# Kernel optimization log

Hardware: AMD Instinct MI355X
Metric: run time of the kernel (lower is better)

Reference implementation:

```python
import jax, jax.numpy as jnp
import numpy as np

B, LQ, LK = 8, 1024, 1024
H, HD = 8, 128            # n_head, hidden_dim (per-head)
HEAD_DIM, CHILD_DIM = 512, 512
D_MODEL = HEAD_DIM + CHILD_DIM
TEMP = float(np.sqrt(HD))
NEG = 100000000.0
EPS = 1e-5


def setup_inputs() -> dict:
    key = jax.random.key(0)
    ks = jax.random.split(key, 12)
    q = jax.random.normal(ks[0], (B, LQ, HEAD_DIM), jnp.float32)
    k = jax.random.normal(ks[1], (B, LK, CHILD_DIM), jnp.float32)
    v = jax.random.normal(ks[2], (B, LK, D_MODEL), jnp.float32)
    old_score = 0.1 * jax.random.normal(ks[3], (H * B, LQ, LK), jnp.float32)
    float_mask = (jax.random.uniform(ks[4], (B, LQ, LK)) > 0.2).astype(jnp.float32)
    # torch nn.Linear weights are [out_features, in_features]
    wq = jax.random.normal(ks[5], (H * HD, HEAD_DIM), jnp.float32) * np.sqrt(2.0 / (HEAD_DIM + HD))
    wk = jax.random.normal(ks[6], (H * HD, CHILD_DIM), jnp.float32) * np.sqrt(2.0 / (CHILD_DIM + HD))
    wv = jax.random.normal(ks[7], (H * HD, D_MODEL), jnp.float32) * np.sqrt(2.0 / (D_MODEL + HD))
    wfc = jax.random.normal(ks[8], (D_MODEL, H * HD), jnp.float32) * np.sqrt(2.0 / (D_MODEL + H * HD))
    bq = jnp.zeros((H * HD,), jnp.float32)
    bk = jnp.zeros((H * HD,), jnp.float32)
    bv = jnp.zeros((H * HD,), jnp.float32)
    bfc = jnp.zeros((D_MODEL,), jnp.float32)
    ln_g = jnp.ones((D_MODEL,), jnp.float32)
    ln_b = jnp.zeros((D_MODEL,), jnp.float32)
    return dict(q=q, k=k, v=v, old_score=old_score, float_mask=float_mask,
                wq=wq, bq=bq, wk=wk, bk=bk, wv=wv, bv=bv,
                wfc=wfc, bfc=bfc, ln_g=ln_g, ln_b=ln_b)


def reference(q, k, v, old_score, float_mask, wq, bq, wk, bk, wv, bv, wfc, bfc, ln_g, ln_b):
    b, lq, _ = q.shape
    lk = k.shape[1]
    residual = v
    qh = (q @ wq.T + bq).reshape(b, lq, H, HD)   # [b,lq,h,d]
    kh = (k @ wk.T + bk).reshape(b, lk, H, HD)
    vh = (v @ wv.T + bv).reshape(b, lk, H, HD)
    # raw_score laid out head-major to match torch's (n_head*B, Lq, Lk)
    raw = jnp.einsum('bqhd,bkhd->hbqk', qh, kh) + old_score.reshape(H, b, lq, lk)
    score = raw - NEG * (1.0 - float_mask)[None]          # broadcast over heads
    attn = jax.nn.softmax(score / TEMP, axis=-1)          # eval path
    out = jnp.einsum('hbqk,bkhd->bqhd', attn, vh).reshape(b, lq, H * HD)
    out = out @ wfc.T + bfc + residual                    # dropout=identity (eval)
    mean = jnp.mean(out, axis=-1, keepdims=True)
    var = jnp.mean(jnp.square(out - mean), axis=-1, keepdims=True)
    out = (out - mean) / jnp.sqrt(var + EPS) * ln_g + ln_b
    return out, raw.reshape(H * b, lq, lk)
```

## Files before the change

kernel.cpp:

```cpp
#include <hip/hip_runtime.h>

typedef unsigned short u16;
typedef __bf16 bf16x8 __attribute__((ext_vector_type(8)));
typedef float f32x4 __attribute__((ext_vector_type(4)));

#define MFMA16(a,b,c) __builtin_amdgcn_mfma_f32_16x16x32_bf16(a,b,c,0,0,0)

static __device__ __forceinline__ u16 f2bf(float f){
  unsigned u = __builtin_bit_cast(unsigned, f);
  u += 0x7fffu + ((u>>16)&1u);
  return (u16)(u>>16);
}
static __device__ __forceinline__ int swz256(int r,int c){ return r*256 + (c ^ ((r&7)<<4)); }
static __device__ __forceinline__ int swz128(int r,int c){ return r*128 + (c ^ ((r&7)<<4)); }

static __device__ __forceinline__ void gload16(const void* g, void* l){
  __builtin_amdgcn_global_load_lds(
      (const __attribute__((address_space(1))) unsigned int*)g,
      (__attribute__((address_space(3))) unsigned int*)l, 16, 0, 0);
}

__global__ void conv_f2b(const float* __restrict__ in, u16* __restrict__ out, int n4){
  int i = blockIdx.x*256 + threadIdx.x;
  if (i >= n4) return;
  float4 f = reinterpret_cast<const float4*>(in)[i];
  ushort4 o; o.x=f2bf(f.x); o.y=f2bf(f.y); o.z=f2bf(f.z); o.w=f2bf(f.w);
  reinterpret_cast<ushort4*>(out)[i] = o;
}

template<int MODE>
__global__ __launch_bounds__(256) void gemm_nt(const u16* __restrict__ A, const u16* __restrict__ Bw,
    const float* __restrict__ bias, const float* __restrict__ resid,
    u16* __restrict__ Cb, float* __restrict__ Cf, int M, int N, int K)
{
  __shared__ uint4 ldsv[2048];
  char* la = (char*)ldsv;
  char* lb = la + 16384;
  const int tid = threadIdx.x, lane = tid&63, w = tid>>6;
  const int l15 = lane&15, l4 = lane>>4;
  const int wm = w&1, wn = w>>1;
  const int mb = blockIdx.x, nb = blockIdx.y;
  const f32x4 zero4 = {0.f,0.f,0.f,0.f};
  f32x4 acc[4][4];
  #pragma unroll
  for (int i=0;i<4;++i)
    #pragma unroll
    for (int j=0;j<4;++j) acc[i][j] = zero4;

  for (int k0=0;k0<K;k0+=64){
    __syncthreads();
    #pragma unroll
    for (int it=0; it<4; ++it){
      int slot = it*256 + tid;
      int r = slot>>3, cg = (slot&7) ^ (r&7);
      gload16(A + (size_t)(mb*128+r)*K + k0 + cg*8, la + (it*256 + w*64)*16);
      gload16(Bw + (size_t)(nb*128+r)*K + k0 + cg*8, lb + (it*256 + w*64)*16);
    }
    __syncthreads();
    #pragma unroll
    for (int kk=0;kk<2;++kk){
      bf16x8 af[4], bfr[4];
      #pragma unroll
      for (int i=0;i<4;++i){
        af[i]  = *reinterpret_cast<const bf16x8*>(la + swz128(wm*64+i*16+l15, (kk*32+l4*8)*2));
        bfr[i] = *reinterpret_cast<const bf16x8*>(lb + swz128(wn*64+i*16+l15, (kk*32+l4*8)*2));
      }
      #pragma unroll
      for (int i=0;i<4;++i)
        #pragma unroll
        for (int j=0;j<4;++j)
          acc[i][j] = MFMA16(af[i], bfr[j], acc[i][j]);
    }
  }
  #pragma unroll
  for (int j=0;j<4;++j){
    int col = nb*128 + wn*64 + j*16 + l15;
    float bv = bias[col];
    #pragma unroll
    for (int i=0;i<4;++i){
      int row0 = mb*128 + wm*64 + i*16 + l4*4;
      if (MODE == 0){
        #pragma unroll
        for (int r=0;r<4;++r)
          Cb[(size_t)(row0+r)*N + col] = f2bf(acc[i][j][r] + bv);
      } else if (MODE == 1){
        int bb = row0 >> 10, kp = row0 & 1023;
        ushort4 o;
        o.x = f2bf(acc[i][j][0]+bv); o.y = f2bf(acc[i][j][1]+bv);
        o.z = f2bf(acc[i][j][2]+bv); o.w = f2bf(acc[i][j][3]+bv);
        *reinterpret_cast<ushort4*>(Cb + (size_t)(bb*1024+col)*1024 + kp) = o;
      } else {
        #pragma unroll
        for (int r=0;r<4;++r){
          size_t off = (size_t)(row0+r)*N + col;
          Cf[off] = acc[i][j][r] + bv + resid[off];
        }
      }
    }
  }
}

__global__ __launch_bounds__(256) void attn_fused(const u16* __restrict__ qh,
    const u16* __restrict__ kh, const u16* __restrict__ vt,
    const float* __restrict__ oldsc, const float* __restrict__ fmask,
    float* __restrict__ raw, u16* __restrict__ ao)
{
  __shared__ uint4 ldsv[4608];
  char* lk0 = (char*)ldsv;
  char* lv0 = lk0 + 16384;
  char* lk1 = lk0 + 32768;
  char* lv1 = lk0 + 49152;
  char* lp_ = lk0 + 65536;
  const int tid = threadIdx.x, lane = tid&63, w = tid>>6;
  const int l15 = lane&15, l4 = lane>>4;
  const int qb = blockIdx.x, b = blockIdx.y, h = blockIdx.z;
  const float invT = 0.088388347648318447f;
  const f32x4 zero4 = {0.f,0.f,0.f,0.f};

  const int qglob = qb*64 + w*16 + l4*4;
  const float* oldp = oldsc + ((size_t)(h*8+b)*1024 + qglob)*1024 + l15*4;
  const float* fmp  = fmask + ((size_t)b*1024 + qglob)*1024 + l15*4;
  float*       rawp = raw   + ((size_t)(h*8+b)*1024 + qglob)*1024 + l15*4;
  const u16* khB = kh + (size_t)b*1024*1024 + h*128;
  const u16* vtB = vt + ((size_t)b*1024 + h*128)*1024;

  bf16x8 qf[4];
  {
    const u16* qp = qh + (size_t)(b*1024 + qb*64 + w*16 + l15)*1024 + h*128 + l4*8;
    #pragma unroll
    for (int kk=0;kk<4;++kk)
      qf[kk] = __builtin_bit_cast(bf16x8, *reinterpret_cast<const uint4*>(qp + kk*32));
  }
  f32x4 oacc[8];
  #pragma unroll
  for (int i=0;i<8;++i) oacc[i] = zero4;
  float mr[4], lr[4];
  #pragma unroll
  for (int r=0;r<4;++r){ mr[r] = -3.0e38f; lr[r] = 0.f; }

  auto stage = [&](int kt, char* lkD, char* lvD){
    #pragma unroll
    for (int it=0; it<4; ++it){
      int slot = it*256 + tid;
      int rs = slot>>4, cs = slot&15;
      int cgk = cs ^ (rs&7);
      int kv = (rs&15)*4 + (rs>>4);
      gload16(khB + (size_t)(kt*64 + kv)*1024 + cgk*8, lkD + (it*256 + w*64)*16);
      int r8 = slot>>3, cgv = (slot&7) ^ (r8&7);
      gload16(vtB + (size_t)r8*1024 + kt*64 + cgv*8, lvD + (it*256 + w*64)*16);
    }
  };
  auto pref = [&](int kt, float4 (&o4)[4], float4 (&m4)[4]){
    #pragma unroll
    for (int r=0;r<4;++r){
      o4[r] = *reinterpret_cast<const float4*>(oldp + (size_t)r*1024 + kt*64);
      m4[r] = *reinterpret_cast<const float4*>(fmp  + (size_t)r*1024 + kt*64);
    }
  };
  auto body = [&](int kt, char* lkR, char* lvR, float4 (&o4)[4], float4 (&m4)[4]){
    f32x4 fs[4];
    #pragma unroll
    for (int fj=0;fj<4;++fj){
      f32x4 s = zero4;
      #pragma unroll
      for (int kk=0;kk<4;++kk){
        bf16x8 kf = *reinterpret_cast<const bf16x8*>(lkR + swz256(fj*16+l15, (kk*32+l4*8)*2));
        s = MFMA16(qf[kk], kf, s);
      }
      fs[fj] = s;
    }
    float tm[4];
    #pragma unroll
    for (int r=0;r<4;++r){
      float4 rv;
      rv.x = fs[0][r] + o4[r].x; rv.y = fs[1][r] + o4[r].y;
      rv.z = fs[2][r] + o4[r].z; rv.w = fs[3][r] + o4[r].w;
      *reinterpret_cast<float4*>(rawp + (size_t)r*1024 + kt*64) = rv;
      fs[0][r] = (rv.x - 1.0e8f*(1.0f - m4[r].x)) * invT;
      fs[1][r] = (rv.y - 1.0e8f*(1.0f - m4[r].y)) * invT;
      fs[2][r] = (rv.z - 1.0e8f*(1.0f - m4[r].z)) * invT;
      fs[3][r] = (rv.w - 1.0e8f*(1.0f - m4[r].w)) * invT;
      tm[r] = fmaxf(fmaxf(fs[0][r], fs[1][r]), fmaxf(fs[2][r], fs[3][r]));
    }
    #pragma unroll
    for (int o=1;o<16;o<<=1){
      #pragma unroll
      for (int r=0;r<4;++r) tm[r] = fmaxf(tm[r], __shfl_xor(tm[r], o));
    }
    #pragma unroll
    for (int r=0;r<4;++r){
      float mn  = fmaxf(mr[r], tm[r]);
      float esc = __expf(mr[r] - mn);
      mr[r] = mn;
      lr[r] *= esc;
      #pragma unroll
      for (int nf=0;nf<8;++nf) oacc[nf][r] *= esc;
      float px = __expf(fs[0][r] - mn), py = __expf(fs[1][r] - mn);
      float pz = __expf(fs[2][r] - mn), pw = __expf(fs[3][r] - mn);
      lr[r] += px + py + pz + pw;
      ushort4 o;
      o.x = f2bf(px); o.y = f2bf(py); o.z = f2bf(pz); o.w = f2bf(pw);
      int prow = w*16 + l4*4 + r;
      *reinterpret_cast<ushort4*>(lp_ + swz128(prow, l15*8)) = o;
    }
    #pragma unroll
    for (int kkv=0;kkv<2;++kkv){
      bf16x8 pf = *reinterpret_cast<const bf16x8*>(lp_ + swz128(w*16+l15, (kkv*32+l4*8)*2));
      #pragma unroll
      for (int nf=0;nf<8;++nf){
        bf16x8 vf = *reinterpret_cast<const bf16x8*>(lvR + swz128(nf*16+l15, (kkv*32+l4*8)*2));
        oacc[nf] = MFMA16(pf, vf, oacc[nf]);
      }
    }
    __syncthreads();
  };

  float4 oA[4], mA[4], oB[4], mB[4];
  stage(0, lk0, lv0);
  pref(0, oA, mA);
  __syncthreads();
  for (int kt=0; kt<16; kt+=2){
    stage(kt+1, lk1, lv1);
    pref(kt+1, oB, mB);
    body(kt, lk0, lv0, oA, mA);
    if (kt+2 < 16){ stage(kt+2, lk0, lv0); pref(kt+2, oA, mA); }
    body(kt+1, lk1, lv1, oB, mB);
  }

  #pragma unroll
  for (int o=1;o<16;o<<=1){
    #pragma unroll
    for (int r=0;r<4;++r) lr[r] += __shfl_xor(lr[r], o);
  }
  #pragma unroll
  for (int nf=0;nf<8;++nf){
    int col = h*128 + nf*16 + l15;
    #pragma unroll
    for (int r=0;r<4;++r){
      size_t orow = (size_t)(b*1024 + qb*64 + w*16 + l4*4 + r);
      ao[orow*1024 + col] = f2bf(oacc[nf][r] * (1.0f/lr[r]));
    }
  }
}

__global__ __launch_bounds__(256) void ln_k(float* __restrict__ io,
    const float* __restrict__ g, const float* __restrict__ bb)
{
  const int lane = threadIdx.x & 63, w = threadIdx.x >> 6;
  size_t row = (size_t)blockIdx.x*4 + w;
  float4* p = reinterpret_cast<float4*>(io + row*1024);
  float4 x[4];
  float s = 0.f, s2 = 0.f;
  #pragma unroll
  for (int i=0;i<4;++i){
    x[i] = p[lane + i*64];
    s  += x[i].x + x[i].y + x[i].z + x[i].w;
    s2 += x[i].x*x[i].x + x[i].y*x[i].y + x[i].z*x[i].z + x[i].w*x[i].w;
  }
  #pragma unroll
  for (int o=1;o<64;o<<=1){ s += __shfl_xor(s,o); s2 += __shfl_xor(s2,o); }
  float mean = s * 0.0009765625f;
  float var  = s2 * 0.0009765625f - mean*mean;
  float rstd = rsqrtf(var + 1e-5f);
  const float4* gp = reinterpret_cast<const float4*>(g);
  const float4* bp = reinterpret_cast<const float4*>(bb);
  #pragma unroll
  for (int i=0;i<4;++i){
    float4 gg = gp[lane+i*64], bv = bp[lane+i*64], y;
    y.x = (x[i].x-mean)*rstd*gg.x + bv.x;
    y.y = (x[i].y-mean)*rstd*gg.y + bv.y;
    y.z = (x[i].z-mean)*rstd*gg.z + bv.z;
    y.w = (x[i].w-mean)*rstd*gg.w + bv.w;
    p[lane+i*64] = y;
  }
}

extern "C" void kernel_launch(void* const* d_in, const int* in_sizes, int n_in,
                              void* d_out, int out_size, void* d_ws, size_t ws_size,
                              hipStream_t stream)
{
  const float* q    = (const float*)d_in[0];
  const float* k    = (const float*)d_in[1];
  const float* v    = (const float*)d_in[2];
  const float* olds = (const float*)d_in[3];
  const float* fm   = (const float*)d_in[4];
  const float* wq   = (const float*)d_in[5];
  const float* bq   = (const float*)d_in[6];
  const float* wk   = (const float*)d_in[7];
  const float* bk   = (const float*)d_in[8];
  const float* wv   = (const float*)d_in[9];
  const float* bv   = (const float*)d_in[10];
  const float* wfc  = (const float*)d_in[11];
  const float* bfc  = (const float*)d_in[12];
  const float* lng  = (const float*)d_in[13];
  const float* lnb  = (const float*)d_in[14];
  float* out = (float*)d_out;
  float* raw = out + 8388608;

  u16* ws  = (u16*)d_ws;
  u16* qbf = ws;
  u16* kbf = qbf + 4194304;
  u16* vbf = kbf + 4194304;
  u16* wqb = vbf + 8388608;
  u16* wkb = wqb + 524288;
  u16* wvb = wkb + 524288;
  u16* wfb = wvb + 1048576;
  u16* qhb = wfb + 1048576;
  u16* khb = qhb + 8388608;
  u16* vtb = khb + 8388608;
  u16* aob = vtb + 8388608;

  conv_f2b<<<4096,256,0,stream>>>(q,   qbf, 1048576);
  conv_f2b<<<4096,256,0,stream>>>(k,   kbf, 1048576);
  conv_f2b<<<8192,256,0,stream>>>(v,   vbf, 2097152);
  conv_f2b<<<512, 256,0,stream>>>(wq,  wqb, 131072);
  conv_f2b<<<512, 256,0,stream>>>(wk,  wkb, 131072);
  conv_f2b<<<1024,256,0,stream>>>(wv,  wvb, 262144);
  conv_f2b<<<1024,256,0,stream>>>(wfc, wfb, 262144);

  gemm_nt<0><<<dim3(64,8),256,0,stream>>>(qbf, wqb, bq, nullptr, qhb, nullptr, 8192,1024,512);
  gemm_nt<0><<<dim3(64,8),256,0,stream>>>(kbf, wkb, bk, nullptr, khb, nullptr, 8192,1024,512);
  gemm_nt<1><<<dim3(64,8),256,0,stream>>>(vbf, wvb, bv, nullptr, vtb, nullptr, 8192,1024,1024);

  attn_fused<<<dim3(16,8,8),256,0,stream>>>(qhb, khb, vtb, olds, fm, raw, aob);

  gemm_nt<2><<<dim3(64,8),256,0,stream>>>(aob, wfb, bfc, v, nullptr, out, 8192,1024,1024);
  ln_k<<<2048,256,0,stream>>>(out, lng, lnb);
}
```

Baseline: 313.2 us.

## Pack attention mask to bits, remap blocks, and pipeline attention with explicit waits

A new kernel packs the float mask into one bit per element, so the attention kernel reads one byte per 8 mask values instead of float4 loads, which cuts mask traffic inside attention. The attention grid becomes 1D, with a block-index remap so blocks sharing the same (b,h) are grouped across XCDs for K/V cache reuse. The main loop is rewritten with explicit vmcnt waits, raw barriers and sched_barriers so the next tile's loads stay in flight while the current tile computes, replacing full __syncthreads. The cost is an extra pass over the mask plus more fragile manual synchronisation.

```diff
diff --git a/kernel.cpp b/kernel.cpp
--- a/kernel.cpp
+++ b/kernel.cpp
@@ -5,6 +5,9 @@
 typedef float f32x4 __attribute__((ext_vector_type(4)));
 
 #define MFMA16(a,b,c) __builtin_amdgcn_mfma_f32_16x16x32_bf16(a,b,c,0,0,0)
+#define WAITV(n) asm volatile("s_waitcnt vmcnt(" #n ")" ::: "memory")
+#define SBAR()   __builtin_amdgcn_s_barrier()
+#define SCHED0() __builtin_amdgcn_sched_barrier(0)
 
 static __device__ __forceinline__ u16 f2bf(float f){
   unsigned u = __builtin_bit_cast(unsigned, f);
@@ -26,6 +29,22 @@
   float4 f = reinterpret_cast<const float4*>(in)[i];
   ushort4 o; o.x=f2bf(f.x); o.y=f2bf(f.y); o.z=f2bf(f.z); o.w=f2bf(f.w);
   reinterpret_cast<ushort4*>(out)[i] = o;
+}
+
+__global__ void mask2bits(const float* __restrict__ fm, unsigned char* __restrict__ bits){
+  int i = blockIdx.x*256 + threadIdx.x;
+  const float4* p = reinterpret_cast<const float4*>(fm + (size_t)i*8);
+  float4 a = p[0], bq = p[1];
+  unsigned v = 0;
+  v |= (a.x  > 0.5f) ? 1u   : 0u;
+  v |= (a.y  > 0.5f) ? 2u   : 0u;
+  v |= (a.z  > 0.5f) ? 4u   : 0u;
+  v |= (a.w  > 0.5f) ? 8u   : 0u;
+  v |= (bq.x > 0.5f) ? 16u  : 0u;
+  v |= (bq.y > 0.5f) ? 32u  : 0u;
+  v |= (bq.z > 0.5f) ? 64u  : 0u;
+  v |= (bq.w > 0.5f) ? 128u : 0u;
+  bits[i] = (unsigned char)v;
 }
 
 template<int MODE>
@@ -102,7 +121,7 @@
 
 __global__ __launch_bounds__(256) void attn_fused(const u16* __restrict__ qh,
     const u16* __restrict__ kh, const u16* __restrict__ vt,
-    const float* __restrict__ oldsc, const float* __restrict__ fmask,
+    const float* __restrict__ oldsc, const unsigned char* __restrict__ bits,
     float* __restrict__ raw, u16* __restrict__ ao)
 {
   __shared__ uint4 ldsv[4608];
@@ -113,16 +132,20 @@
   char* lp_ = lk0 + 65536;
   const int tid = threadIdx.x, lane = tid&63, w = tid>>6;
   const int l15 = lane&15, l4 = lane>>4;
-  const int qb = blockIdx.x, b = blockIdx.y, h = blockIdx.z;
+  unsigned ublk = blockIdx.x;
+  int slotid = (ublk & 7) * 128 + (ublk >> 3);
+  const int qb = slotid & 15, bh = slotid >> 4;
+  const int b = bh & 7, h = bh >> 3;
   const float invT = 0.088388347648318447f;
   const f32x4 zero4 = {0.f,0.f,0.f,0.f};
 
   const int qglob = qb*64 + w*16 + l4*4;
   const float* oldp = oldsc + ((size_t)(h*8+b)*1024 + qglob)*1024 + l15*4;
-  const float* fmp  = fmask + ((size_t)b*1024 + qglob)*1024 + l15*4;
   float*       rawp = raw   + ((size_t)(h*8+b)*1024 + qglob)*1024 + l15*4;
+  const unsigned char* bitp = bits + ((size_t)b*1024 + qglob)*128 + (l15>>1);
   const u16* khB = kh + (size_t)b*1024*1024 + h*128;
   const u16* vtB = vt + ((size_t)b*1024 + h*128)*1024;
+  const int nsh = (l15&1)*4;
 
   bf16x8 qf[4];
   {
@@ -143,21 +166,21 @@
     for (int it=0; it<4; ++it){
       int slot = it*256 + tid;
       int rs = slot>>4, cs = slot&15;
-      int cgk = cs ^ (rs&7);
+      int ck = cs ^ (rs&7);
       int kv = (rs&15)*4 + (rs>>4);
-      gload16(khB + (size_t)(kt*64 + kv)*1024 + cgk*8, lkD + (it*256 + w*64)*16);
+      gload16(khB + (size_t)(kt*64 + kv)*1024 + ck*8, lkD + (it*256 + w*64)*16);
       int r8 = slot>>3, cgv = (slot&7) ^ (r8&7);
       gload16(vtB + (size_t)r8*1024 + kt*64 + cgv*8, lvD + (it*256 + w*64)*16);
     }
   };
-  auto pref = [&](int kt, float4 (&o4)[4], float4 (&m4)[4]){
+  auto pref = [&](int kt, float4 (&o4)[4], unsigned char (&bb)[4]){
     #pragma unroll
     for (int r=0;r<4;++r){
       o4[r] = *reinterpret_cast<const float4*>(oldp + (size_t)r*1024 + kt*64);
-      m4[r] = *reinterpret_cast<const float4*>(fmp  + (size_t)r*1024 + kt*64);
+      bb[r] = bitp[(size_t)r*128 + kt*8];
     }
   };
-  auto body = [&](int kt, char* lkR, char* lvR, float4 (&o4)[4], float4 (&m4)[4]){
+  auto body = [&](int kt, char* lkR, char* lvR, float4 (&o4)[4], unsigned char (&bb)[4]){
     f32x4 fs[4];
     #pragma unroll
     for (int fj=0;fj<4;++fj){
@@ -176,10 +199,11 @@
       rv.x = fs[0][r] + o4[r].x; rv.y = fs[1][r] + o4[r].y;
       rv.z = fs[2][r] + o4[r].z; rv.w = fs[3][r] + o4[r].w;
       *reinterpret_cast<float4*>(rawp + (size_t)r*1024 + kt*64) = rv;
-      fs[0][r] = (rv.x - 1.0e8f*(1.0f - m4[r].x)) * invT;
-      fs[1][r] = (rv.y - 1.0e8f*(1.0f - m4[r].y)) * invT;
-      fs[2][r] = (rv.z - 1.0e8f*(1.0f - m4[r].z)) * invT;
-      fs[3][r] = (rv.w - 1.0e8f*(1.0f - m4[r].w)) * invT;
+      unsigned nib = ((unsigned)bb[r]) >> nsh;
+      fs[0][r] = (rv.x - ((nib&1u) ? 0.f : 1.0e8f)) * invT;
+      fs[1][r] = (rv.y - ((nib&2u) ? 0.f : 1.0e8f)) * invT;
+      fs[2][r] = (rv.z - ((nib&4u) ? 0.f : 1.0e8f)) * invT;
+      fs[3][r] = (rv.w - ((nib&8u) ? 0.f : 1.0e8f)) * invT;
       tm[r] = fmaxf(fmaxf(fs[0][r], fs[1][r]), fmaxf(fs[2][r], fs[3][r]));
     }
     #pragma unroll
@@ -212,20 +236,38 @@
         oacc[nf] = MFMA16(pf, vf, oacc[nf]);
       }
     }
-    __syncthreads();
   };
 
-  float4 oA[4], mA[4], oB[4], mB[4];
+  float4 oA[4], oB[4];
+  unsigned char bA[4], bB[4];
   stage(0, lk0, lv0);
-  pref(0, oA, mA);
-  __syncthreads();
-  for (int kt=0; kt<16; kt+=2){
-    stage(kt+1, lk1, lv1);
-    pref(kt+1, oB, mB);
-    body(kt, lk0, lv0, oA, mA);
-    if (kt+2 < 16){ stage(kt+2, lk0, lv0); pref(kt+2, oA, mA); }
-    body(kt+1, lk1, lv1, oB, mB);
-  }
+  stage(1, lk1, lv1);
+  pref(0, oA, bA);
+  pref(1, oB, bB);
+  WAITV(8);
+  SBAR(); SCHED0();
+  body(0, lk0, lv0, oA, bA);
+  pref(2, oA, bA);
+
+  #pragma unroll 1
+  for (int t = 1; t <= 13; t += 2){
+    SBAR();
+    stage(t+1, lk0, lv0);
+    WAITV(16);
+    SBAR(); SCHED0();
+    body(t, lk1, lv1, oB, bB);
+    if (t+2 <= 15) pref(t+2, oB, bB);
+    SBAR();
+    stage(t+2, lk1, lv1);
+    WAITV(16);
+    SBAR(); SCHED0();
+    body(t+1, lk0, lv0, oA, bA);
+    if (t+3 <= 15) pref(t+3, oA, bA);
+  }
+  SBAR();
+  WAITV(0);
+  SBAR(); SCHED0();
+  body(15, lk1, lv1, oB, bB);
 
   #pragma unroll
   for (int o=1;o<16;o<<=1){
@@ -309,6 +351,7 @@
   u16* khb = qhb + 8388608;
   u16* vtb = khb + 8388608;
   u16* aob = vtb + 8388608;
+  unsigned char* bits = (unsigned char*)(aob + 8388608);
 
   conv_f2b<<<4096,256,0,stream>>>(q,   qbf, 1048576);
   conv_f2b<<<4096,256,0,stream>>>(k,   kbf, 1048576);
@@ -317,12 +360,13 @@
   conv_f2b<<<512, 256,0,stream>>>(wk,  wkb, 131072);
   conv_f2b<<<1024,256,0,stream>>>(wv,  wvb, 262144);
   conv_f2b<<<1024,256,0,stream>>>(wfc, wfb, 262144);
+  mask2bits<<<4096,256,0,stream>>>(fm, bits);
 
   gemm_nt<0><<<dim3(64,8),256,0,stream>>>(qbf, wqb, bq, nullptr, qhb, nullptr, 8192,1024,512);
   gemm_nt<0><<<dim3(64,8),256,0,stream>>>(kbf, wkb, bk, nullptr, khb, nullptr, 8192,1024,512);
   gemm_nt<1><<<dim3(64,8),256,0,stream>>>(vbf, wvb, bv, nullptr, vtb, nullptr, 8192,1024,1024);
 
-  attn_fused<<<dim3(16,8,8),256,0,stream>>>(qhb, khb, vtb, olds, fm, raw, aob);
+  attn_fused<<<1024,256,0,stream>>>(qhb, khb, vtb, olds, bits, raw, aob);
 
   gemm_nt<2><<<dim3(64,8),256,0,stream>>>(aob, wfb, bfc, v, nullptr, out, 8192,1024,1024);
   ln_k<<<2048,256,0,stream>>>(out, lng, lnb);
```

After: 303.4 us. -3.1%, faster.
